# Optimization experiments

Measured on AMD Instinct MI355X. Metric: run time of the kernel, lower is better.

## Reference

```python
import jax, jax.numpy as jnp
import numpy as np

N_NODES = 50000
N_EDGES = 800000
IN_C, HID_C, OUT_C = 128, 128, 64


def setup_inputs() -> dict:
    key = jax.random.key(0)
    ks = jax.random.split(key, 8)
    x = jax.random.normal(ks[0], (N_NODES, IN_C), dtype=jnp.float32)
    edge_index = jax.random.randint(ks[1], (2, N_EDGES), 0, N_NODES, dtype=jnp.int32)
    edge_weight = jax.random.uniform(ks[2], (N_EDGES,), dtype=jnp.float32)
    node_type = jax.random.randint(ks[3], (N_NODES,), 0, 4, dtype=jnp.int32)
    s1 = 1.0 / np.sqrt(IN_C)
    s2 = 1.0 / np.sqrt(HID_C)
    return {
        "x": x,
        "edge_index": edge_index,
        "edge_weight": edge_weight,
        "node_type": node_type,
        "W_l1": jax.random.normal(ks[4], (HID_C, IN_C), dtype=jnp.float32) * s1,
        "b_l1": jnp.zeros((HID_C,), dtype=jnp.float32),
        "W_r1": jax.random.normal(ks[5], (HID_C, IN_C), dtype=jnp.float32) * s1,
        "W_l2": jax.random.normal(ks[6], (OUT_C, HID_C), dtype=jnp.float32) * s2,
        "b_l2": jnp.zeros((OUT_C,), dtype=jnp.float32),
        "W_r2": jax.random.normal(ks[7], (OUT_C, HID_C), dtype=jnp.float32) * s2,
    }


def _sage_conv(h, src, dst, edge_weight, W_l, b_l, W_r, num_nodes):
    # message: edge_weight * x_src, mean-aggregated at dst (PyG SAGEConv mean aggr)
    msg = h[src] * edge_weight[:, None]                                  # [E, C]
    agg = jax.ops.segment_sum(msg, dst, num_segments=num_nodes)          # [N, C]
    deg = jax.ops.segment_sum(jnp.ones_like(edge_weight), dst, num_segments=num_nodes)
    agg = agg / jnp.maximum(deg, 1.0)[:, None]
    # out = lin_l(agg) + lin_r(root); bias only on lin_l (PyG convention)
    return agg @ W_l.T + b_l + h @ W_r.T


def reference(x, edge_index, edge_weight, node_type, W_l1, b_l1, W_r1, W_l2, b_l2, W_r2):
    num_nodes = x.shape[0]
    src, dst = edge_index[0], edge_index[1]
    h = _sage_conv(x, src, dst, edge_weight, W_l1, b_l1, W_r1, num_nodes)
    h = jax.nn.relu(h)  # dropout p=0.0 -> identity
    out = _sage_conv(h, src, dst, edge_weight, W_l2, b_l2, W_r2, num_nodes)
    return out
```

## Files before the change

kernel.cpp:

```cpp
#include <hip/hip_runtime.h>

constexpr int IN_C  = 128;
constexpr int HID_C = 128;
constexpr int OUT_C = 64;

constexpr int BSHIFT    = 7;
constexpr int NBUCK_MAX = 512;
constexpr int CAP       = 4096;
constexpr int EPB       = 4096;

typedef short bf16x8 __attribute__((ext_vector_type(8)));
typedef float f32x4  __attribute__((ext_vector_type(4)));
typedef float f32x2  __attribute__((ext_vector_type(2)));

__device__ __forceinline__ unsigned short f2b(float f) {
    unsigned u = __float_as_uint(f);
    unsigned r = (u + 0x7fffu + ((u >> 16) & 1u)) >> 16;
    return (unsigned short)r;
}
__device__ __forceinline__ float b2f_lo(unsigned u) { return __uint_as_float(u << 16); }
__device__ __forceinline__ float b2f_hi(unsigned u) { return __uint_as_float(u & 0xffff0000u); }
__device__ __forceinline__ unsigned char f2fp8(float f) {
    int p = __builtin_amdgcn_cvt_pk_fp8_f32(f, f, 0, false);
    return (unsigned char)(p & 0xff);
}

struct Acc8 {
    float a0 = 0, a1 = 0, a2 = 0, a3 = 0, a4 = 0, a5 = 0, a6 = 0, a7 = 0;
    __device__ __forceinline__ void acc_fp8(uint2 v, float wt) {
        f32x2 p0 = __builtin_amdgcn_cvt_pk_f32_fp8(v.x, false);
        f32x2 p1 = __builtin_amdgcn_cvt_pk_f32_fp8(v.x, true);
        f32x2 p2 = __builtin_amdgcn_cvt_pk_f32_fp8(v.y, false);
        f32x2 p3 = __builtin_amdgcn_cvt_pk_f32_fp8(v.y, true);
        a0 = fmaf(p0[0], wt, a0); a1 = fmaf(p0[1], wt, a1);
        a2 = fmaf(p1[0], wt, a2); a3 = fmaf(p1[1], wt, a3);
        a4 = fmaf(p2[0], wt, a4); a5 = fmaf(p2[1], wt, a5);
        a6 = fmaf(p3[0], wt, a6); a7 = fmaf(p3[1], wt, a7);
    }
    __device__ __forceinline__ void acc_bf16(uint4 v, float wt) {
        a0 = fmaf(b2f_lo(v.x), wt, a0); a1 = fmaf(b2f_hi(v.x), wt, a1);
        a2 = fmaf(b2f_lo(v.y), wt, a2); a3 = fmaf(b2f_hi(v.y), wt, a3);
        a4 = fmaf(b2f_lo(v.z), wt, a4); a5 = fmaf(b2f_hi(v.z), wt, a5);
        a6 = fmaf(b2f_lo(v.w), wt, a6); a7 = fmaf(b2f_hi(v.w), wt, a7);
    }
};


__global__ __launch_bounds__(256) void k_init(
    int* __restrict__ bcnt, int NBUCK,
    const float* __restrict__ wa, const float* __restrict__ wb,
    const float* __restrict__ wc, const float* __restrict__ wd,
    unsigned short* __restrict__ wab, unsigned short* __restrict__ wbb,
    unsigned short* __restrict__ wcb, unsigned short* __restrict__ wdb) {
    if (blockIdx.x == 0) {
        for (int i = threadIdx.x; i < NBUCK; i += 256) bcnt[i] = 0;
        return;
    }
    const int NW1 = HID_C * IN_C, NW3 = OUT_C * HID_C;
    int off = ((blockIdx.x - 1) * 256 + threadIdx.x) * 4;
    if (off >= 2 * NW1 + 2 * NW3) return;
    const float* s; unsigned short* d;
    if (off < NW1) { s = wa; d = wab; }
    else { off -= NW1;
        if (off < NW1) { s = wb; d = wbb; }
        else { off -= NW1;
            if (off < NW3) { s = wc; d = wcb; }
            else { off -= NW3; s = wd; d = wdb; }
        }
    }
    float4 v = *reinterpret_cast<const float4*>(s + off);
    ushort4 o;
    o.x = f2b(v.x); o.y = f2b(v.y); o.z = f2b(v.z); o.w = f2b(v.w);
    *reinterpret_cast<ushort4*>(d + off) = o;
}


__device__ __forceinline__ void gemm1_body(
    int bx, const float* __restrict__ A, const unsigned short* __restrict__ Wm,
    const unsigned short* __restrict__ Wr, unsigned char* __restrict__ Om,
    unsigned short* __restrict__ Or, int N) {
    constexpr int K = IN_C;
    int wave = threadIdx.x >> 6;
    int lane = threadIdx.x & 63;
    int tile = bx * 4 + wave;
    int m0 = tile * 16;
    if (m0 >= N) return;
    int lm = lane & 15;
    int quad = lane >> 4;
    int row = min(m0 + lm, N - 1);

    bf16x8 afrag[K / 32];
#pragma unroll
    for (int kk = 0; kk < K / 32; kk++) {
        const float* ap = A + (size_t)row * K + kk * 32 + quad * 8;
        float4 u0 = *reinterpret_cast<const float4*>(ap);
        float4 u1 = *reinterpret_cast<const float4*>(ap + 4);
        bf16x8 a;
        a[0] = (short)f2b(u0.x); a[1] = (short)f2b(u0.y);
        a[2] = (short)f2b(u0.z); a[3] = (short)f2b(u0.w);
        a[4] = (short)f2b(u1.x); a[5] = (short)f2b(u1.y);
        a[6] = (short)f2b(u1.z); a[7] = (short)f2b(u1.w);
        afrag[kk] = a;
    }
#pragma unroll
    for (int j = 0; j < HID_C / 16; j++) {
        const unsigned short* wrow = Wm + (size_t)(j * 16 + lm) * K + quad * 8;
        f32x4 acc = {0.f, 0.f, 0.f, 0.f};
#pragma unroll
        for (int kk = 0; kk < K / 32; kk++) {
            bf16x8 b = *reinterpret_cast<const bf16x8*>(wrow + kk * 32);
            acc = __builtin_amdgcn_mfma_f32_16x16x32_bf16(afrag[kk], b, acc, 0, 0, 0);
        }
#pragma unroll
        for (int r = 0; r < 4; r++) {
            int node = m0 + quad * 4 + r;
            if (node < N) Om[(size_t)node * HID_C + j * 16 + lm] = f2fp8(acc[r]);
        }
    }
#pragma unroll
    for (int j = 0; j < HID_C / 16; j++) {
        const unsigned short* wrow = Wr + (size_t)(j * 16 + lm) * K + quad * 8;
        f32x4 acc = {0.f, 0.f, 0.f, 0.f};
#pragma unroll
        for (int kk = 0; kk < K / 32; kk++) {
            bf16x8 b = *reinterpret_cast<const bf16x8*>(wrow + kk * 32);
            acc = __builtin_amdgcn_mfma_f32_16x16x32_bf16(afrag[kk], b, acc, 0, 0, 0);
        }
#pragma unroll
        for (int r = 0; r < 4; r++) {
            int node = m0 + quad * 4 + r;
            if (node < N) Or[(size_t)node * HID_C + j * 16 + lm] = f2b(acc[r]);
        }
    }
}


__global__ __launch_bounds__(256) void k_fill_gemm1(
    const int* __restrict__ src, const int* __restrict__ dst,
    const float* __restrict__ ew, int E, int NBUCK, int EBLK,
    int* __restrict__ bcnt, int2* __restrict__ brec,
    const float* __restrict__ x, const unsigned short* __restrict__ wl1b,
    const unsigned short* __restrict__ wr1b, unsigned char* __restrict__ msg1,
    unsigned short* __restrict__ root1, int N) {
    if (blockIdx.x >= EBLK) {
        gemm1_body(blockIdx.x - EBLK, x, wl1b, wr1b, msg1, root1, N);
        return;
    }
    __shared__ int lh[NBUCK_MAX], lbase[NBUCK_MAX], lcnt[NBUCK_MAX];
    for (int i = threadIdx.x; i < NBUCK; i += 256) { lh[i] = 0; lcnt[i] = 0; }
    __syncthreads();
    int base = blockIdx.x * EPB;
#pragma unroll 4
    for (int i = 0; i < EPB / 256; i++) {
        int e = base + i * 256 + threadIdx.x;
        if (e < E) atomicAdd(&lh[dst[e] >> BSHIFT], 1);
    }
    __syncthreads();
    for (int i = threadIdx.x; i < NBUCK; i += 256) {
        int v = lh[i];
        lbase[i] = v ? (i * CAP + atomicAdd(&bcnt[i], v)) : 0;
    }
    __syncthreads();
#pragma unroll 4
    for (int i = 0; i < EPB / 256; i++) {
        int e = base + i * 256 + threadIdx.x;
        if (e < E) {
            int d = dst[e];
            int b = d >> BSHIFT;
            int loc = atomicAdd(&lcnt[b], 1);
            int2 r;
            r.x = __float_as_int(ew[e]);
            r.y = (src[e] & 0xffff) | ((d & 127) << 16);
            brec[(size_t)lbase[b] + loc] = r;
        }
    }
}

__global__ __launch_bounds__(256) void k_bcsr(const int2* __restrict__ brec,
                                              const int* __restrict__ bcnt, int N,
                                              int2* __restrict__ row_range,
                                              unsigned int* __restrict__ csr) {
    __shared__ int lh[128], lex[128], lcnt[128], sc[128];
    int b = blockIdx.x, t = threadIdx.x;
    if (t < 128) { lh[t] = 0; lcnt[t] = 0; }
    __syncthreads();
    int beg = b * CAP;
    int cnt = bcnt[b];
    for (int e = t; e < cnt; e += 256)
        atomicAdd(&lh[(brec[beg + e].y >> 16) & 127], 1);
    __syncthreads();
    if (t < 128) sc[t] = lh[t];
    __syncthreads();
    for (int d = 1; d < 128; d <<= 1) {
        int v = (t >= d && t < 128) ? sc[t - d] : 0;
        __syncthreads();
        if (t < 128) sc[t] += v;
        __syncthreads();
    }
    if (t < 128) lex[t] = sc[t] - lh[t];
    __syncthreads();
    int node_base = b << BSHIFT;
    if (t < 128 && node_base + t < N)
        row_range[node_base + t] = make_int2(beg + lex[t], beg + sc[t]);
    for (int e = t; e < cnt; e += 256) {
        int2 r = brec[beg + e];
        int d = (r.y >> 16) & 127;
        int loc = atomicAdd(&lcnt[d], 1);
        unsigned int w16 = (unsigned int)f2b(__int_as_float(r.x)) << 16;
        csr[(size_t)beg + lex[d] + loc] = (unsigned int)(r.y & 0xffff) | w16;
    }
}


constexpr int HSTRIDE = HID_C + 8;

__global__ __launch_bounds__(256) void k_comb1_gemm2(
    const unsigned char* __restrict__ msg1,
    const unsigned short* __restrict__ root1,
    const float* __restrict__ b1,
    const int2* __restrict__ row_range, const unsigned int* __restrict__ crec,
    const unsigned short* __restrict__ wl2b,
    const unsigned short* __restrict__ wr2b,
    unsigned short* __restrict__ msg2,
    unsigned short* __restrict__ root2,
    int N) {
    __shared__ unsigned short hls[16 * HSTRIDE];
    int tid = threadIdx.x;
    int nl = tid >> 4;
    int m0 = blockIdx.x * 16;
    int node = m0 + nl;
    int c8 = (tid & 15) * 8;
    bool valid = node < N;

    int beg = 0, end = 0;
    if (valid) { int2 rr = row_range[node]; beg = rr.x; end = rr.y; }

    Acc8 ac;
    int e = beg;
    for (; e + 3 < end; e += 4) {
        unsigned int r0e = crec[e],     r1e = crec[e + 1];
        unsigned int r2e = crec[e + 2], r3e = crec[e + 3];
        float w0 = b2f_hi(r0e), w1 = b2f_hi(r1e);
        float w2 = b2f_hi(r2e), w3 = b2f_hi(r3e);
        uint2 v0 = *reinterpret_cast<const uint2*>(msg1 + (size_t)(r0e & 0xffff) * HID_C + c8);
        uint2 v1 = *reinterpret_cast<const uint2*>(msg1 + (size_t)(r1e & 0xffff) * HID_C + c8);
        uint2 v2 = *reinterpret_cast<const uint2*>(msg1 + (size_t)(r2e & 0xffff) * HID_C + c8);
        uint2 v3 = *reinterpret_cast<const uint2*>(msg1 + (size_t)(r3e & 0xffff) * HID_C + c8);
        ac.acc_fp8(v0, w0); ac.acc_fp8(v1, w1);
        ac.acc_fp8(v2, w2); ac.acc_fp8(v3, w3);
    }
    for (; e < end; e++) {
        unsigned int r0e = crec[e];
        uint2 v0 = *reinterpret_cast<const uint2*>(msg1 + (size_t)(r0e & 0xffff) * HID_C + c8);
        ac.acc_fp8(v0, b2f_hi(r0e));
    }
    uint4 pk = {0, 0, 0, 0};
    if (valid) {
        float inv = 1.0f / fmaxf((float)(end - beg), 1.0f);
        uint4 rv = *reinterpret_cast<const uint4*>(root1 + (size_t)node * HID_C + c8);
        float4 b0 = *reinterpret_cast<const float4*>(b1 + c8);
        float4 b1v = *reinterpret_cast<const float4*>(b1 + c8 + 4);
        float o0 = fmaxf(fmaf(ac.a0, inv, b0.x + b2f_lo(rv.x)), 0.f);
        float o1 = fmaxf(fmaf(ac.a1, inv, b0.y + b2f_hi(rv.x)), 0.f);
        float o2 = fmaxf(fmaf(ac.a2, inv, b0.z + b2f_lo(rv.y)), 0.f);
        float o3 = fmaxf(fmaf(ac.a3, inv, b0.w + b2f_hi(rv.y)), 0.f);
        float o4 = fmaxf(fmaf(ac.a4, inv, b1v.x + b2f_lo(rv.z)), 0.f);
        float o5 = fmaxf(fmaf(ac.a5, inv, b1v.y + b2f_hi(rv.z)), 0.f);
        float o6 = fmaxf(fmaf(ac.a6, inv, b1v.z + b2f_lo(rv.w)), 0.f);
        float o7 = fmaxf(fmaf(ac.a7, inv, b1v.w + b2f_hi(rv.w)), 0.f);
        pk.x = (unsigned)f2b(o0) | ((unsigned)f2b(o1) << 16);
        pk.y = (unsigned)f2b(o2) | ((unsigned)f2b(o3) << 16);
        pk.z = (unsigned)f2b(o4) | ((unsigned)f2b(o5) << 16);
        pk.w = (unsigned)f2b(o6) | ((unsigned)f2b(o7) << 16);
    }
    *reinterpret_cast<uint4*>(&hls[nl * HSTRIDE + c8]) = pk;
    __syncthreads();

    int wave = tid >> 6;
    int lane = tid & 63;
    int lm = lane & 15;
    int quad = lane >> 4;

    bf16x8 afrag[4];
#pragma unroll
    for (int kk = 0; kk < 4; kk++)
        afrag[kk] = *reinterpret_cast<const bf16x8*>(&hls[lm * HSTRIDE + kk * 32 + quad * 8]);

#pragma unroll
    for (int t = 0; t < 2; t++) {
        int jt = wave * 2 + t;
        const unsigned short* W = (jt < 4) ? wl2b : wr2b;
        unsigned short* O = (jt < 4) ? msg2 : root2;
        int j = jt & 3;
        const unsigned short* wrow = W + (size_t)(j * 16 + lm) * HID_C + quad * 8;
        f32x4 acc = {0.f, 0.f, 0.f, 0.f};
#pragma unroll
        for (int kk = 0; kk < 4; kk++) {
            bf16x8 b = *reinterpret_cast<const bf16x8*>(wrow + kk * 32);
            acc = __builtin_amdgcn_mfma_f32_16x16x32_bf16(afrag[kk], b, acc, 0, 0, 0);
        }
#pragma unroll
        for (int r = 0; r < 4; r++) {
            int nd = m0 + quad * 4 + r;
            if (nd < N) O[(size_t)nd * OUT_C + j * 16 + lm] = f2b(acc[r]);
        }
    }
}


__global__ __launch_bounds__(256) void k_combine2(
    const unsigned short* __restrict__ msg2,
    const unsigned short* __restrict__ root2,
    const float* __restrict__ bias,
    const int2* __restrict__ row_range, const unsigned int* __restrict__ crec,
    float* __restrict__ out, int N) {
    constexpr int C = OUT_C;
    constexpr int LPN = C / 8;
    constexpr int NPB = 256 / LPN;
    int tid = threadIdx.x;
    int node = blockIdx.x * NPB + tid / LPN;
    if (node >= N) return;
    int c8 = (tid % LPN) * 8;
    int2 rr = row_range[node];
    int beg = rr.x, end = rr.y;

    Acc8 ac;
    int e = beg;
    for (; e + 3 < end; e += 4) {
        unsigned int r0e = crec[e],     r1e = crec[e + 1];
        unsigned int r2e = crec[e + 2], r3e = crec[e + 3];
        uint4 v0 = *reinterpret_cast<const uint4*>(msg2 + (size_t)(r0e & 0xffff) * C + c8);
        uint4 v1 = *reinterpret_cast<const uint4*>(msg2 + (size_t)(r1e & 0xffff) * C + c8);
        uint4 v2 = *reinterpret_cast<const uint4*>(msg2 + (size_t)(r2e & 0xffff) * C + c8);
        uint4 v3 = *reinterpret_cast<const uint4*>(msg2 + (size_t)(r3e & 0xffff) * C + c8);
        ac.acc_bf16(v0, b2f_hi(r0e)); ac.acc_bf16(v1, b2f_hi(r1e));
        ac.acc_bf16(v2, b2f_hi(r2e)); ac.acc_bf16(v3, b2f_hi(r3e));
    }
    for (; e < end; e++) {
        unsigned int r0e = crec[e];
        uint4 v0 = *reinterpret_cast<const uint4*>(msg2 + (size_t)(r0e & 0xffff) * C + c8);
        ac.acc_bf16(v0, b2f_hi(r0e));
    }
    float inv = 1.0f / fmaxf((float)(end - beg), 1.0f);
    uint4 rv = *reinterpret_cast<const uint4*>(root2 + (size_t)node * C + c8);
    float4 b0 = *reinterpret_cast<const float4*>(bias + c8);
    float4 b1 = *reinterpret_cast<const float4*>(bias + c8 + 4);
    float* op = out + (size_t)node * C + c8;
    *reinterpret_cast<float4*>(op) = make_float4(
        fmaf(ac.a0, inv, b0.x + b2f_lo(rv.x)), fmaf(ac.a1, inv, b0.y + b2f_hi(rv.x)),
        fmaf(ac.a2, inv, b0.z + b2f_lo(rv.y)), fmaf(ac.a3, inv, b0.w + b2f_hi(rv.y)));
    *reinterpret_cast<float4*>(op + 4) = make_float4(
        fmaf(ac.a4, inv, b1.x + b2f_lo(rv.z)), fmaf(ac.a5, inv, b1.y + b2f_hi(rv.z)),
        fmaf(ac.a6, inv, b1.z + b2f_lo(rv.w)), fmaf(ac.a7, inv, b1.w + b2f_hi(rv.w)));
}


extern "C" void kernel_launch(void* const* d_in, const int* in_sizes, int n_in,
                              void* d_out, int out_size, void* d_ws, size_t ws_size,
                              hipStream_t stream) {
    const float* x    = (const float*)d_in[0];
    const int*   eidx = (const int*)d_in[1];
    const float* ew   = (const float*)d_in[2];
    const float* W_l1 = (const float*)d_in[4];
    const float* b_l1 = (const float*)d_in[5];
    const float* W_r1 = (const float*)d_in[6];
    const float* W_l2 = (const float*)d_in[7];
    const float* b_l2 = (const float*)d_in[8];
    const float* W_r2 = (const float*)d_in[9];
    float* out = (float*)d_out;

    const int N = in_sizes[0] / IN_C;
    const int E = in_sizes[1] / 2;
    const int* src = eidx;
    const int* dst = eidx + E;
    const int NBUCK = (N + 127) >> BSHIFT;
    const int EBLK = (E + EPB - 1) / EPB;
    const int WBLK = ((2 * HID_C * IN_C + 2 * OUT_C * HID_C) / 4 + 255) / 256;

    char* p = (char*)d_ws;
    auto carve = [&](size_t bytes) -> char* {
        char* r = p;
        p += (bytes + 255) & ~(size_t)255;
        return r;
    };
    int*  bcnt      = (int*)carve((size_t)NBUCK * 4);
    int2* row_range = (int2*)carve((size_t)N * 8);
    int2* brec      = (int2*)carve((size_t)NBUCK * CAP * 8);
    unsigned int* csr = (unsigned int*)carve((size_t)NBUCK * CAP * 4);
    unsigned short* wl1b = (unsigned short*)carve((size_t)HID_C * IN_C * 2);
    unsigned short* wr1b = (unsigned short*)carve((size_t)HID_C * IN_C * 2);
    unsigned short* wl2b = (unsigned short*)carve((size_t)OUT_C * HID_C * 2);
    unsigned short* wr2b = (unsigned short*)carve((size_t)OUT_C * HID_C * 2);
    unsigned char*  msg1 = (unsigned char*)carve((size_t)N * HID_C);
    unsigned short* root1 = (unsigned short*)carve((size_t)N * HID_C * 2);
    unsigned short* msg2 = (unsigned short*)carve((size_t)N * OUT_C * 2);
    unsigned short* root2 = (unsigned short*)carve((size_t)N * OUT_C * 2);

    int tiles = (N + 15) / 16;
    int gblk = (tiles + 3) / 4;

    k_init<<<1 + WBLK, 256, 0, stream>>>(bcnt, NBUCK,
        W_l1, W_r1, W_l2, W_r2, wl1b, wr1b, wl2b, wr2b);
    k_fill_gemm1<<<EBLK + gblk, 256, 0, stream>>>(
        src, dst, ew, E, NBUCK, EBLK, bcnt, brec,
        x, wl1b, wr1b, msg1, root1, N);
    k_bcsr<<<NBUCK, 256, 0, stream>>>(brec, bcnt, N, row_range, csr);
    k_comb1_gemm2<<<tiles, 256, 0, stream>>>(
        msg1, root1, b_l1, row_range, csr, wl2b, wr2b, msg2, root2, N);
    k_combine2<<<(N + 31) / 32, 256, 0, stream>>>(
        msg2, root2, b_l2, row_range, csr, out, N);
}
```

Measured before the change: 187.6 us.

## Fuse bucket CSR build into layer-1 combine and layer-2 GEMM kernel

Merges the per-bucket CSR construction kernel with the layer-1 aggregation plus layer-2 GEMM kernel, so each block builds its bucket's CSR in shared memory and consumes it directly instead of reading it back from global memory. Bucket size is halved to 64 nodes (capacity 2048) so the CSR and the hidden tile fit in LDS. This removes one launch and a global CSR round trip for layer 1, while CSR and row ranges are still written out for layer 2. In exchange, launches drop from about 3125 blocks to about 782, with roughly 26 KB of LDS per block, which may reduce occupancy and latency hiding on the gather. The smaller capacity also risks overflow if a 64-node bucket receives more than 2048 edges.

```diff
diff --git a/kernel.cpp b/kernel.cpp
--- a/kernel.cpp
+++ b/kernel.cpp
@@ -4,9 +4,10 @@
 constexpr int HID_C = 128;
 constexpr int OUT_C = 64;
 
-constexpr int BSHIFT    = 7;
-constexpr int NBUCK_MAX = 512;
-constexpr int CAP       = 4096;
+constexpr int BSHIFT    = 6;
+constexpr int BNODES    = 64;
+constexpr int NBUCK_MAX = 1024;
+constexpr int CAP       = 2048;
 constexpr int EPB       = 4096;
 
 typedef short bf16x8 __attribute__((ext_vector_type(8)));
@@ -170,139 +171,134 @@
             int loc = atomicAdd(&lcnt[b], 1);
             int2 r;
             r.x = __float_as_int(ew[e]);
-            r.y = (src[e] & 0xffff) | ((d & 127) << 16);
+            r.y = (src[e] & 0xffff) | ((d & (BNODES - 1)) << 16);
             brec[(size_t)lbase[b] + loc] = r;
         }
     }
 }
 
-__global__ __launch_bounds__(256) void k_bcsr(const int2* __restrict__ brec,
-                                              const int* __restrict__ bcnt, int N,
-                                              int2* __restrict__ row_range,
-                                              unsigned int* __restrict__ csr) {
-    __shared__ int lh[128], lex[128], lcnt[128], sc[128];
+
+constexpr int HSTRIDE = HID_C + 8;
+
+__global__ __launch_bounds__(256) void k_csr_comb_gemm2(
+    const int2* __restrict__ brec, const int* __restrict__ bcnt, int N,
+    int2* __restrict__ row_range, unsigned int* __restrict__ csr,
+    const unsigned char* __restrict__ msg1,
+    const unsigned short* __restrict__ root1,
+    const float* __restrict__ b1,
+    const unsigned short* __restrict__ wl2b,
+    const unsigned short* __restrict__ wr2b,
+    unsigned short* __restrict__ msg2,
+    unsigned short* __restrict__ root2) {
+    __shared__ int lh[BNODES], lex[BNODES], lsc[BNODES], lcnt[BNODES];
+    __shared__ unsigned int lcsr[CAP];
+    __shared__ unsigned short hls[BNODES * HSTRIDE];
     int b = blockIdx.x, t = threadIdx.x;
-    if (t < 128) { lh[t] = 0; lcnt[t] = 0; }
+    if (t < BNODES) { lh[t] = 0; lcnt[t] = 0; }
     __syncthreads();
     int beg = b * CAP;
     int cnt = bcnt[b];
     for (int e = t; e < cnt; e += 256)
-        atomicAdd(&lh[(brec[beg + e].y >> 16) & 127], 1);
-    __syncthreads();
-    if (t < 128) sc[t] = lh[t];
-    __syncthreads();
-    for (int d = 1; d < 128; d <<= 1) {
-        int v = (t >= d && t < 128) ? sc[t - d] : 0;
+        atomicAdd(&lh[(brec[beg + e].y >> 16) & (BNODES - 1)], 1);
+    __syncthreads();
+    if (t < BNODES) lsc[t] = lh[t];
+    __syncthreads();
+    for (int d = 1; d < BNODES; d <<= 1) {
+        int v = (t >= d && t < BNODES) ? lsc[t - d] : 0;
         __syncthreads();
-        if (t < 128) sc[t] += v;
+        if (t < BNODES) lsc[t] += v;
         __syncthreads();
     }
-    if (t < 128) lex[t] = sc[t] - lh[t];
+    if (t < BNODES) lex[t] = lsc[t] - lh[t];
     __syncthreads();
     int node_base = b << BSHIFT;
-    if (t < 128 && node_base + t < N)
-        row_range[node_base + t] = make_int2(beg + lex[t], beg + sc[t]);
+    if (t < BNODES && node_base + t < N)
+        row_range[node_base + t] = make_int2(beg + lex[t], beg + lsc[t]);
     for (int e = t; e < cnt; e += 256) {
         int2 r = brec[beg + e];
-        int d = (r.y >> 16) & 127;
+        int d = (r.y >> 16) & (BNODES - 1);
         int loc = atomicAdd(&lcnt[d], 1);
-        unsigned int w16 = (unsigned int)f2b(__int_as_float(r.x)) << 16;
-        csr[(size_t)beg + lex[d] + loc] = (unsigned int)(r.y & 0xffff) | w16;
-    }
-}
-
-
-constexpr int HSTRIDE = HID_C + 8;
-
-__global__ __launch_bounds__(256) void k_comb1_gemm2(
-    const unsigned char* __restrict__ msg1,
-    const unsigned short* __restrict__ root1,
-    const float* __restrict__ b1,
-    const int2* __restrict__ row_range, const unsigned int* __restrict__ crec,
-    const unsigned short* __restrict__ wl2b,
-    const unsigned short* __restrict__ wr2b,
-    unsigned short* __restrict__ msg2,
-    unsigned short* __restrict__ root2,
-    int N) {
-    __shared__ unsigned short hls[16 * HSTRIDE];
-    int tid = threadIdx.x;
-    int nl = tid >> 4;
-    int m0 = blockIdx.x * 16;
-    int node = m0 + nl;
-    int c8 = (tid & 15) * 8;
-    bool valid = node < N;
-
-    int beg = 0, end = 0;
-    if (valid) { int2 rr = row_range[node]; beg = rr.x; end = rr.y; }
-
-    Acc8 ac;
-    int e = beg;
-    for (; e + 3 < end; e += 4) {
-        unsigned int r0e = crec[e],     r1e = crec[e + 1];
-        unsigned int r2e = crec[e + 2], r3e = crec[e + 3];
-        float w0 = b2f_hi(r0e), w1 = b2f_hi(r1e);
-        float w2 = b2f_hi(r2e), w3 = b2f_hi(r3e);
-        uint2 v0 = *reinterpret_cast<const uint2*>(msg1 + (size_t)(r0e & 0xffff) * HID_C + c8);
-        uint2 v1 = *reinterpret_cast<const uint2*>(msg1 + (size_t)(r1e & 0xffff) * HID_C + c8);
-        uint2 v2 = *reinterpret_cast<const uint2*>(msg1 + (size_t)(r2e & 0xffff) * HID_C + c8);
-        uint2 v3 = *reinterpret_cast<const uint2*>(msg1 + (size_t)(r3e & 0xffff) * HID_C + c8);
-        ac.acc_fp8(v0, w0); ac.acc_fp8(v1, w1);
-        ac.acc_fp8(v2, w2); ac.acc_fp8(v3, w3);
-    }
-    for (; e < end; e++) {
-        unsigned int r0e = crec[e];
-        uint2 v0 = *reinterpret_cast<const uint2*>(msg1 + (size_t)(r0e & 0xffff) * HID_C + c8);
-        ac.acc_fp8(v0, b2f_hi(r0e));
-    }
-    uint4 pk = {0, 0, 0, 0};
-    if (valid) {
-        float inv = 1.0f / fmaxf((float)(end - beg), 1.0f);
-        uint4 rv = *reinterpret_cast<const uint4*>(root1 + (size_t)node * HID_C + c8);
-        float4 b0 = *reinterpret_cast<const float4*>(b1 + c8);
-        float4 b1v = *reinterpret_cast<const float4*>(b1 + c8 + 4);
-        float o0 = fmaxf(fmaf(ac.a0, inv, b0.x + b2f_lo(rv.x)), 0.f);
-        float o1 = fmaxf(fmaf(ac.a1, inv, b0.y + b2f_hi(rv.x)), 0.f);
-        float o2 = fmaxf(fmaf(ac.a2, inv, b0.z + b2f_lo(rv.y)), 0.f);
-        float o3 = fmaxf(fmaf(ac.a3, inv, b0.w + b2f_hi(rv.y)), 0.f);
-        float o4 = fmaxf(fmaf(ac.a4, inv, b1v.x + b2f_lo(rv.z)), 0.f);
-        float o5 = fmaxf(fmaf(ac.a5, inv, b1v.y + b2f_hi(rv.z)), 0.f);
-        float o6 = fmaxf(fmaf(ac.a6, inv, b1v.z + b2f_lo(rv.w)), 0.f);
-        float o7 = fmaxf(fmaf(ac.a7, inv, b1v.w + b2f_hi(rv.w)), 0.f);
-        pk.x = (unsigned)f2b(o0) | ((unsigned)f2b(o1) << 16);
-        pk.y = (unsigned)f2b(o2) | ((unsigned)f2b(o3) << 16);
-        pk.z = (unsigned)f2b(o4) | ((unsigned)f2b(o5) << 16);
-        pk.w = (unsigned)f2b(o6) | ((unsigned)f2b(o7) << 16);
-    }
-    *reinterpret_cast<uint4*>(&hls[nl * HSTRIDE + c8]) = pk;
-    __syncthreads();
-
-    int wave = tid >> 6;
-    int lane = tid & 63;
+        lcsr[lex[d] + loc] =
+            (unsigned)(r.y & 0xffff) | ((unsigned)f2b(__int_as_float(r.x)) << 16);
+    }
+    __syncthreads();
+    for (int e = t; e < cnt; e += 256) csr[beg + e] = lcsr[e];
+    int c8 = (t & 15) * 8;
+#pragma unroll
+    for (int g = 0; g < BNODES / 16; g++) {
+        int nl = g * 16 + (t >> 4);
+        int node = node_base + nl;
+        bool valid = node < N;
+        int eb = lex[nl], ee = lsc[nl];
+        Acc8 ac;
+        int e = eb;
+        for (; e + 3 < ee; e += 4) {
+            unsigned int r0e = lcsr[e],     r1e = lcsr[e + 1];
+            unsigned int r2e = lcsr[e + 2], r3e = lcsr[e + 3];
+            uint2 v0 = *reinterpret_cast<const uint2*>(msg1 + (size_t)(r0e & 0xffff) * HID_C + c8);
+            uint2 v1 = *reinterpret_cast<const uint2*>(msg1 + (size_t)(r1e & 0xffff) * HID_C + c8);
+            uint2 v2 = *reinterpret_cast<const uint2*>(msg1 + (size_t)(r2e & 0xffff) * HID_C + c8);
+            uint2 v3 = *reinterpret_cast<const uint2*>(msg1 + (size_t)(r3e & 0xffff) * HID_C + c8);
+            ac.acc_fp8(v0, b2f_hi(r0e)); ac.acc_fp8(v1, b2f_hi(r1e));
+            ac.acc_fp8(v2, b2f_hi(r2e)); ac.acc_fp8(v3, b2f_hi(r3e));
+        }
+        for (; e < ee; e++) {
+            unsigned int r0e = lcsr[e];
+            uint2 v0 = *reinterpret_cast<const uint2*>(msg1 + (size_t)(r0e & 0xffff) * HID_C + c8);
+            ac.acc_fp8(v0, b2f_hi(r0e));
+        }
+        uint4 pk = {0, 0, 0, 0};
+        if (valid) {
+            float inv = 1.0f / fmaxf((float)(ee - eb), 1.0f);
+            uint4 rv = *reinterpret_cast<const uint4*>(root1 + (size_t)node * HID_C + c8);
+            float4 b0 = *reinterpret_cast<const float4*>(b1 + c8);
+            float4 b1v = *reinterpret_cast<const float4*>(b1 + c8 + 4);
+            float o0 = fmaxf(fmaf(ac.a0, inv, b0.x + b2f_lo(rv.x)), 0.f);
+            float o1 = fmaxf(fmaf(ac.a1, inv, b0.y + b2f_hi(rv.x)), 0.f);
+            float o2 = fmaxf(fmaf(ac.a2, inv, b0.z + b2f_lo(rv.y)), 0.f);
+            float o3 = fmaxf(fmaf(ac.a3, inv, b0.w + b2f_hi(rv.y)), 0.f);
+            float o4 = fmaxf(fmaf(ac.a4, inv, b1v.x + b2f_lo(rv.z)), 0.f);
+            float o5 = fmaxf(fmaf(ac.a5, inv, b1v.y + b2f_hi(rv.z)), 0.f);
+            float o6 = fmaxf(fmaf(ac.a6, inv, b1v.z + b2f_lo(rv.w)), 0.f);
+            float o7 = fmaxf(fmaf(ac.a7, inv, b1v.w + b2f_hi(rv.w)), 0.f);
+            pk.x = (unsigned)f2b(o0) | ((unsigned)f2b(o1) << 16);
+            pk.y = (unsigned)f2b(o2) | ((unsigned)f2b(o3) << 16);
+            pk.z = (unsigned)f2b(o4) | ((unsigned)f2b(o5) << 16);
+            pk.w = (unsigned)f2b(o6) | ((unsigned)f2b(o7) << 16);
+        }
+        *reinterpret_cast<uint4*>(&hls[nl * HSTRIDE + c8]) = pk;
+    }
+    __syncthreads();
+    int wave = t >> 6;
+    int lane = t & 63;
     int lm = lane & 15;
     int quad = lane >> 4;
-
-    bf16x8 afrag[4];
-#pragma unroll
-    for (int kk = 0; kk < 4; kk++)
-        afrag[kk] = *reinterpret_cast<const bf16x8*>(&hls[lm * HSTRIDE + kk * 32 + quad * 8]);
-
-#pragma unroll
-    for (int t = 0; t < 2; t++) {
-        int jt = wave * 2 + t;
-        const unsigned short* W = (jt < 4) ? wl2b : wr2b;
-        unsigned short* O = (jt < 4) ? msg2 : root2;
-        int j = jt & 3;
-        const unsigned short* wrow = W + (size_t)(j * 16 + lm) * HID_C + quad * 8;
-        f32x4 acc = {0.f, 0.f, 0.f, 0.f};
-#pragma unroll
-        for (int kk = 0; kk < 4; kk++) {
-            bf16x8 b = *reinterpret_cast<const bf16x8*>(wrow + kk * 32);
-            acc = __builtin_amdgcn_mfma_f32_16x16x32_bf16(afrag[kk], b, acc, 0, 0, 0);
-        }
-#pragma unroll
-        for (int r = 0; r < 4; r++) {
-            int nd = m0 + quad * 4 + r;
-            if (nd < N) O[(size_t)nd * OUT_C + j * 16 + lm] = f2b(acc[r]);
+#pragma unroll
+    for (int mt = 0; mt < BNODES / 16; mt++) {
+        int m0 = node_base + mt * 16;
+        bf16x8 afrag[4];
+#pragma unroll
+        for (int kk = 0; kk < 4; kk++)
+            afrag[kk] = *reinterpret_cast<const bf16x8*>(
+                &hls[(mt * 16 + lm) * HSTRIDE + kk * 32 + quad * 8]);
+#pragma unroll
+        for (int t2 = 0; t2 < 2; t2++) {
+            int jt = wave * 2 + t2;
+            const unsigned short* W = (jt < 4) ? wl2b : wr2b;
+            unsigned short* O = (jt < 4) ? msg2 : root2;
+            int j = jt & 3;
+            const unsigned short* wrow = W + (size_t)(j * 16 + lm) * HID_C + quad * 8;
+            f32x4 acc = {0.f, 0.f, 0.f, 0.f};
+#pragma unroll
+            for (int kk = 0; kk < 4; kk++) {
+                bf16x8 bb = *reinterpret_cast<const bf16x8*>(wrow + kk * 32);
+                acc = __builtin_amdgcn_mfma_f32_16x16x32_bf16(afrag[kk], bb, acc, 0, 0, 0);
+            }
+#pragma unroll
+            for (int r = 0; r < 4; r++) {
+                int nd = m0 + quad * 4 + r;
+                if (nd < N) O[(size_t)nd * OUT_C + j * 16 + lm] = f2b(acc[r]);
+            }
         }
     }
 }
@@ -373,7 +369,7 @@
     const int E = in_sizes[1] / 2;
     const int* src = eidx;
     const int* dst = eidx + E;
-    const int NBUCK = (N + 127) >> BSHIFT;
+    const int NBUCK = (N + BNODES - 1) >> BSHIFT;
     const int EBLK = (E + EPB - 1) / EPB;
     const int WBLK = ((2 * HID_C * IN_C + 2 * OUT_C * HID_C) / 4 + 255) / 256;
 
@@ -404,9 +400,9 @@
     k_fill_gemm1<<<EBLK + gblk, 256, 0, stream>>>(
         src, dst, ew, E, NBUCK, EBLK, bcnt, brec,
         x, wl1b, wr1b, msg1, root1, N);
-    k_bcsr<<<NBUCK, 256, 0, stream>>>(brec, bcnt, N, row_range, csr);
-    k_comb1_gemm2<<<tiles, 256, 0, stream>>>(
-        msg1, root1, b_l1, row_range, csr, wl2b, wr2b, msg2, root2, N);
+    k_csr_comb_gemm2<<<NBUCK, 256, 0, stream>>>(
+        brec, bcnt, N, row_range, csr, msg1, root1, b_l1,
+        wl2b, wr2b, msg2, root2);
     k_combine2<<<(N + 31) / 32, 256, 0, stream>>>(
         msg2, root2, b_l2, row_range, csr, out, N);
 }
```

After: 170.4 us. -9.2%, faster.
